# Kernel tuning notes

Measured on AMD Instinct MI355X. Metric: run time of the kernel, lower is better.

## Reference

```python
import jax, jax.numpy as jnp
import numpy as np

N = 20000          # nodes
E = 320000         # directed edges (self-loops added in reference)
F_IN = 128         # input node features
HEADS = 8
HID = 64           # per-head hidden channels
G = 64             # graphs in the batch
NUM_CLASSES = 10
NEG_SLOPE = 0.2    # PyG GATConv LeakyReLU slope


def _gat_layer(x, src, dst, W, a_src, a_dst, bias, n_nodes):
    """PyG-style GATConv: messages flow src->dst, softmax over incoming edges."""
    H, C = a_src.shape
    h = (x @ W).reshape(n_nodes, H, C)                     # [N,H,C]
    asrc = jnp.einsum('nhc,hc->nh', h, a_src)              # [N,H]
    adst = jnp.einsum('nhc,hc->nh', h, a_dst)              # [N,H]
    e = jax.nn.leaky_relu(asrc[src] + adst[dst], NEG_SLOPE)  # [Etot,H]
    emax = jax.ops.segment_max(e, dst, num_segments=n_nodes)  # [N,H]
    ee = jnp.exp(e - emax[dst])
    denom = jax.ops.segment_sum(ee, dst, num_segments=n_nodes)
    alpha = ee / (denom[dst] + 1e-16)                      # [Etot,H]
    out = jax.ops.segment_sum(h[src] * alpha[:, :, None], dst, num_segments=n_nodes)
    return out.reshape(n_nodes, H * C) + bias


def setup_inputs() -> dict:
    key = jax.random.key(0)
    ks = jax.random.split(key, 10)
    x = jax.random.normal(ks[0], (N, F_IN), jnp.float32)
    edge_index = jax.random.randint(ks[1], (2, E), 0, N, jnp.int32)
    batch = jnp.sort(jax.random.randint(ks[2], (N,), 0, G, jnp.int32))
    # layer 1: F_IN -> HEADS*HID (concat)
    W1 = jax.random.normal(ks[3], (F_IN, HEADS * HID), jnp.float32) / np.float32(np.sqrt(F_IN))
    a_src1 = jax.random.normal(ks[4], (HEADS, HID), jnp.float32) / np.float32(np.sqrt(HID))
    a_dst1 = jax.random.normal(ks[5], (HEADS, HID), jnp.float32) / np.float32(np.sqrt(HID))
    b1 = jnp.zeros((HEADS * HID,), jnp.float32)
    # layer 2: HEADS*HID -> NUM_CLASSES (1 head)
    W2 = jax.random.normal(ks[6], (HEADS * HID, NUM_CLASSES), jnp.float32) / np.float32(np.sqrt(HEADS * HID))
    a_src2 = jax.random.normal(ks[7], (1, NUM_CLASSES), jnp.float32) / np.float32(np.sqrt(NUM_CLASSES))
    a_dst2 = jax.random.normal(ks[8], (1, NUM_CLASSES), jnp.float32) / np.float32(np.sqrt(NUM_CLASSES))
    b2 = jnp.zeros((NUM_CLASSES,), jnp.float32)
    return {"x": x, "edge_index": edge_index, "batch": batch,
            "W1": W1, "a_src1": a_src1, "a_dst1": a_dst1, "b1": b1,
            "W2": W2, "a_src2": a_src2, "a_dst2": a_dst2, "b2": b2}


def reference(x, edge_index, batch, W1, a_src1, a_dst1, b1, W2, a_src2, a_dst2, b2):
    n = x.shape[0]
    loop = jnp.arange(n, dtype=edge_index.dtype)   # add_self_loops=True (PyG default)
    src = jnp.concatenate([edge_index[0], loop])
    dst = jnp.concatenate([edge_index[1], loop])
    h = jax.nn.elu(_gat_layer(x, src, dst, W1, a_src1, a_dst1, b1, n))
    h = _gat_layer(h, src, dst, W2, a_src2, a_dst2, b2, n)
    # PowerMeanAggregation with default p=1.0 == mean pooling per graph
    sums = jax.ops.segment_sum(h, batch, num_segments=G)                    # [G,NC]
    counts = jax.ops.segment_sum(jnp.ones((n, 1), h.dtype), batch, num_segments=G)
    return sums / jnp.maximum(counts, 1.0)
```

## Files before the change

kernel.cpp:

```cpp
#include <hip/hip_runtime.h>
#include <hip/hip_bf16.h>

typedef unsigned short ushort_t;
typedef unsigned int uint_t;
typedef unsigned char uchar_t;

typedef __attribute__((ext_vector_type(8))) short bf16x8;
typedef __attribute__((ext_vector_type(4))) float f32x4;
typedef __attribute__((ext_vector_type(2))) float f32x2;

__device__ __forceinline__ float bf2f(ushort_t u) {
    union { uint_t i; float f; } v; v.i = ((uint_t)u) << 16; return v.f;
}
__device__ __forceinline__ ushort_t f2bf(float f) {
    __hip_bfloat16 h = __float2bfloat16(f);
    ushort_t u; __builtin_memcpy(&u, &h, 2); return u;
}
__device__ __forceinline__ float leaky(float v) { return (v > 0.f) ? v : 0.2f * v; }

#define PO_AS1 0
#define PO_AD1 512
#define PO_B1  1024
#define PO_W2  1536
#define PO_AS2 6656
#define PO_AD2 6666
#define PO_B2  6676
#define PTOT   6686

__device__ __forceinline__ bool detect_fp32_local(const ushort_t* __restrict__ xa) {
    __shared__ int cnt;
    if (threadIdx.x == 0) cnt = 0;
    __syncthreads();
    int bad = 0;
    for (int i = threadIdx.x; i < 4096; i += 256) {
        float v = bf2f(xa[i]);
        if (!(fabsf(v) < 1e4f)) bad++;
    }
    if (bad) atomicAdd(&cnt, bad);
    __syncthreads();
    return cnt >= 16;
}

__global__ __launch_bounds__(256) void k_prep(const void* __restrict__ x,
                                              const void* __restrict__ W1,
                                              const void* as1, const void* ad1,
                                              const void* b1, const void* W2,
                                              const void* as2, const void* ad2,
                                              const void* b2,
                                              ushort_t* __restrict__ W1t,
                                              float* __restrict__ prm,
                                              float* __restrict__ vab,
                                              int* __restrict__ deg,
                                              float* __restrict__ gacc,
                                              int* __restrict__ flag, int N) {
    int b = blockIdx.x, t = threadIdx.x;
    if (b < 283) {
        bool isf = detect_fp32_local((const ushort_t*)x);
        if (b == 0 && t == 0) *flag = isf ? 1 : 0;
        if (b < 256) {
            int idx = b * 256 + t;
            int n = idx & 511, k = idx >> 9;
            float v = isf ? ((const float*)W1)[k * 512 + n]
                          : bf2f(((const ushort_t*)W1)[k * 512 + n]);
            W1t[n * 128 + k] = f2bf(v);
        } else {
            int i = (b - 256) * 256 + t;
            if (i < PTOT) {
                const void* src; int off;
                if (i < 512)       { src = as1; off = i; }
                else if (i < 1024) { src = ad1; off = i - 512; }
                else if (i < 1536) { src = b1;  off = i - 1024; }
                else if (i < 6656) { src = W2;  off = i - 1536; }
                else if (i < 6666) { src = as2; off = i - 6656; }
                else if (i < 6676) { src = ad2; off = i - 6666; }
                else               { src = b2;  off = i - 6676; }
                prm[i] = isf ? ((const float*)src)[off] : bf2f(((const ushort_t*)src)[off]);
            }
        }
    } else if (b < 362) {
        int i = (b - 283) * 256 + t;
        if (i < N) deg[i] = 0;
    } else if (b == 362) {
        for (int i = t; i < 768; i += 256) gacc[i] = 0.f;
    } else {
        bool isf = detect_fp32_local((const ushort_t*)x);
        int idx = (b - 363) * 256 + t;
        int k = idx >> 4, q = idx & 15;
        int h = q & 7;
        const void* av = (q < 8) ? as1 : ad1;
        float s = 0.f;
        for (int c = 0; c < 64; ++c) {
            float wv = isf ? ((const float*)W1)[k * 512 + h * 64 + c]
                           : bf2f(((const ushort_t*)W1)[k * 512 + h * 64 + c]);
            float aval = isf ? ((const float*)av)[h * 64 + c]
                             : bf2f(((const ushort_t*)av)[h * 64 + c]);
            s += wv * aval;
        }
        vab[k * 16 + q] = s;
    }
}

__global__ __launch_bounds__(256) void k_logits_hist(const void* __restrict__ xraw,
                                                     const float* __restrict__ vab,
                                                     const int* __restrict__ ei,
                                                     const int* __restrict__ flag,
                                                     uchar_t* __restrict__ xq,
                                                     float* __restrict__ asrcf,
                                                     float* __restrict__ adstf,
                                                     int* __restrict__ deg,
                                                     int E, int Etot) {
    int b = blockIdx.x, t = threadIdx.x;
    if (b >= 1250) {
        int e = (b - 1250) * 256 + t;
        if (e < Etot) {
            int dst = (e < E) ? ei[E + e] : (e - E);
            atomicAdd(&deg[dst], 1);
        }
        return;
    }
    bool isf = (*flag != 0);
    int n = b * 16 + (t >> 4);
    int l = t & 15;
    int ch0 = l * 8;
    float xf[8];
    if (isf) {
        const float4* x4 = (const float4*)xraw + (size_t)n * 32 + l * 2;
        float4 f0 = x4[0], f1 = x4[1];
        xf[0] = f0.x; xf[1] = f0.y; xf[2] = f0.z; xf[3] = f0.w;
        xf[4] = f1.x; xf[5] = f1.y; xf[6] = f1.z; xf[7] = f1.w;
    } else {
        uint4 u = ((const uint4*)((const ushort_t*)xraw + (size_t)n * 128))[l];
        xf[0] = bf2f(u.x & 0xffff); xf[1] = bf2f(u.x >> 16);
        xf[2] = bf2f(u.y & 0xffff); xf[3] = bf2f(u.y >> 16);
        xf[4] = bf2f(u.z & 0xffff); xf[5] = bf2f(u.z >> 16);
        xf[6] = bf2f(u.w & 0xffff); xf[7] = bf2f(u.w >> 16);
    }
    uint_t u0 = (uint_t)__builtin_amdgcn_cvt_pk_fp8_f32(xf[0], xf[1], 0, false);
    u0 = (uint_t)__builtin_amdgcn_cvt_pk_fp8_f32(xf[2], xf[3], (int)u0, true);
    uint_t u1 = (uint_t)__builtin_amdgcn_cvt_pk_fp8_f32(xf[4], xf[5], 0, false);
    u1 = (uint_t)__builtin_amdgcn_cvt_pk_fp8_f32(xf[6], xf[7], (int)u1, true);
    uint2 st; st.x = u0; st.y = u1;
    *((uint2*)(xq + (size_t)n * 128) + l) = st;
    float ps[8], pd[8];
#pragma unroll
    for (int h = 0; h < 8; ++h) { ps[h] = 0.f; pd[h] = 0.f; }
#pragma unroll
    for (int j = 0; j < 8; ++j) {
        const float4* vr = (const float4*)&vab[(ch0 + j) * 16];
        float4 va0 = vr[0], va1 = vr[1], vb0 = vr[2], vb1 = vr[3];
        float xv = xf[j];
        ps[0] += xv * va0.x; ps[1] += xv * va0.y; ps[2] += xv * va0.z; ps[3] += xv * va0.w;
        ps[4] += xv * va1.x; ps[5] += xv * va1.y; ps[6] += xv * va1.z; ps[7] += xv * va1.w;
        pd[0] += xv * vb0.x; pd[1] += xv * vb0.y; pd[2] += xv * vb0.z; pd[3] += xv * vb0.w;
        pd[4] += xv * vb1.x; pd[5] += xv * vb1.y; pd[6] += xv * vb1.z; pd[7] += xv * vb1.w;
    }
#pragma unroll
    for (int off = 1; off <= 8; off <<= 1) {
#pragma unroll
        for (int h = 0; h < 8; ++h) {
            ps[h] += __shfl_xor(ps[h], off, 64);
            pd[h] += __shfl_xor(pd[h], off, 64);
        }
    }
    if (l == 0) {
#pragma unroll
        for (int h = 0; h < 8; ++h) {
            asrcf[n * 8 + h] = ps[h];
            adstf[n * 8 + h] = pd[h];
        }
    }
}

__global__ __launch_bounds__(256) void k_scan(const int* __restrict__ deg,
                                              int* __restrict__ rowptr,
                                              int* __restrict__ cursor, int N) {
    int b = blockIdx.x, t = threadIdx.x;
    int lane = t & 63, wv = t >> 6;
    __shared__ int ws[4], wt[4];
    __shared__ int sbase;
    int limit = b * 256;
    int p0 = 0, p1 = 0, p2 = 0, p3 = 0;
    int i = t;
    for (; i + 768 < limit; i += 1024) {
        p0 += deg[i]; p1 += deg[i + 256]; p2 += deg[i + 512]; p3 += deg[i + 768];
    }
    for (; i < limit; i += 256) p0 += deg[i];
    int partial = (p0 + p1) + (p2 + p3);
#pragma unroll
    for (int off = 32; off; off >>= 1) partial += __shfl_xor(partial, off, 64);
    if (lane == 0) ws[wv] = partial;
    __syncthreads();
    if (t == 0) sbase = ws[0] + ws[1] + ws[2] + ws[3];
    __syncthreads();
    int base = sbase;
    i = limit + t;
    int v = (i < N) ? deg[i] : 0;
    int inc = v;
#pragma unroll
    for (int off = 1; off < 64; off <<= 1) {
        int u = __shfl_up(inc, off, 64);
        if (lane >= off) inc += u;
    }
    if (lane == 63) wt[wv] = inc;
    __syncthreads();
    int woff = 0;
    for (int w = 0; w < 4; ++w) if (w < wv) woff += wt[w];
    int excl = base + woff + inc - v;
    if (i < N) { rowptr[i + 1] = excl + v; cursor[i] = excl; }
    if (i == 0) rowptr[0] = 0;
}

__global__ __launch_bounds__(256) void k_scatter(const int* __restrict__ ei,
                                                 int* __restrict__ cursor,
                                                 const float* __restrict__ asrcf,
                                                 const float* __restrict__ adstf,
                                                 int* __restrict__ csr_src,
                                                 float* __restrict__ wcsr,
                                                 int E, int Etot) {
    int e = blockIdx.x * 256 + threadIdx.x;
    if (e >= Etot) return;
    int src, dst;
    if (e < E) { src = ei[e]; dst = ei[E + e]; } else { src = dst = e - E; }
    int pos = atomicAdd(&cursor[dst], 1);
    csr_src[pos] = src;
    const float4* ap = (const float4*)&asrcf[(size_t)src * 8];
    const float4* bp = (const float4*)&adstf[(size_t)dst * 8];
    float4 a0 = ap[0], a1 = ap[1];
    float4 b0 = bp[0], b1 = bp[1];
    float4 w0, w1;
    w0.x = __expf(leaky(a0.x + b0.x));
    w0.y = __expf(leaky(a0.y + b0.y));
    w0.z = __expf(leaky(a0.z + b0.z));
    w0.w = __expf(leaky(a0.w + b0.w));
    w1.x = __expf(leaky(a1.x + b1.x));
    w1.y = __expf(leaky(a1.y + b1.y));
    w1.z = __expf(leaky(a1.z + b1.z));
    w1.w = __expf(leaky(a1.w + b1.w));
    float4* wp = (float4*)&wcsr[(size_t)pos * 8];
    wp[0] = w0; wp[1] = w1;
}

__global__ __launch_bounds__(256) void k_aggfused(const uchar_t* __restrict__ xq,
                                                  const int* __restrict__ rowptr,
                                                  const int* __restrict__ csr_src,
                                                  const float* __restrict__ wcsr,
                                                  const ushort_t* __restrict__ w1t,
                                                  const float* __restrict__ prm,
                                                  ushort_t* __restrict__ h2,
                                                  float* __restrict__ asrc2f,
                                                  float* __restrict__ adst2f) {
    __shared__ ushort_t sA[16 * 1040];
    int b = blockIdx.x, t = threadIdx.x;
    int m0 = b * 16;
    int wave = t >> 6, lane = t & 63;
    for (int mm = 0; mm < 4; ++mm) {
        int mloc = wave * 4 + mm;
        int n = m0 + mloc;
        int start = rowptr[n], end = rowptr[n + 1];
        float acc[16];
        float den[8];
#pragma unroll
        for (int i = 0; i < 16; ++i) acc[i] = 0.f;
#pragma unroll
        for (int h = 0; h < 8; ++h) den[h] = 0.f;
        for (int base = start; base < end; base += 64) {
            int mcap = min(64, end - base);
            int sIdx = csr_src[base + min(lane, mcap - 1)];
            for (int g = 0; g < mcap; g += 4) {
                int s[4]; float4 wA[4], wB[4]; ushort_t xv[4];
#pragma unroll
                for (int j = 0; j < 4; ++j)
                    s[j] = __shfl(sIdx, min(g + j, mcap - 1), 64);
#pragma unroll
                for (int j = 0; j < 4; ++j) {
                    const float4* wp = (const float4*)&wcsr[(size_t)(base + min(g + j, mcap - 1)) * 8];
                    wA[j] = wp[0]; wB[j] = wp[1];
                }
#pragma unroll
                for (int j = 0; j < 4; ++j)
                    xv[j] = *(const ushort_t*)&xq[(size_t)s[j] * 128 + lane * 2];
#pragma unroll
                for (int j = 0; j < 4; ++j) {
                    float msk = (g + j < mcap) ? 1.f : 0.f;
                    f32x2 q = __builtin_amdgcn_cvt_pk_f32_fp8((int)xv[j], false);
                    float w0 = wA[j].x * msk, w1 = wA[j].y * msk, w2 = wA[j].z * msk, w3 = wA[j].w * msk;
                    float w4 = wB[j].x * msk, w5 = wB[j].y * msk, w6 = wB[j].z * msk, w7 = wB[j].w * msk;
                    den[0] += w0; acc[0]  += w0 * q.x; acc[1]  += w0 * q.y;
                    den[1] += w1; acc[2]  += w1 * q.x; acc[3]  += w1 * q.y;
                    den[2] += w2; acc[4]  += w2 * q.x; acc[5]  += w2 * q.y;
                    den[3] += w3; acc[6]  += w3 * q.x; acc[7]  += w3 * q.y;
                    den[4] += w4; acc[8]  += w4 * q.x; acc[9]  += w4 * q.y;
                    den[5] += w5; acc[10] += w5 * q.x; acc[11] += w5 * q.y;
                    den[6] += w6; acc[12] += w6 * q.x; acc[13] += w6 * q.y;
                    den[7] += w7; acc[14] += w7 * q.x; acc[15] += w7 * q.y;
                }
            }
        }
#pragma unroll
        for (int h = 0; h < 8; ++h) {
            float inv = 1.f / (den[h] + 1e-16f);
            uint_t u = (uint_t)f2bf(acc[2 * h] * inv) | ((uint_t)f2bf(acc[2 * h + 1] * inv) << 16);
            *(uint_t*)&sA[mloc * 1040 + h * 128 + 2 * lane] = u;
        }
    }
    __syncthreads();
    int mr = lane & 15, quad = lane >> 4;
    int n0 = wave * 128;
    f32x4 acc2[8];
#pragma unroll
    for (int ct = 0; ct < 8; ++ct) acc2[ct] = {0.f, 0.f, 0.f, 0.f};
#pragma unroll
    for (int kk = 0; kk < 4; ++kk) {
        bf16x8 a0 = *reinterpret_cast<const bf16x8*>(
            &sA[mr * 1040 + (wave * 2) * 128 + quad * 8 + kk * 32]);
        bf16x8 a1 = *reinterpret_cast<const bf16x8*>(
            &sA[mr * 1040 + (wave * 2 + 1) * 128 + quad * 8 + kk * 32]);
#pragma unroll
        for (int ct = 0; ct < 8; ++ct) {
            bf16x8 bb = *reinterpret_cast<const bf16x8*>(
                &w1t[(size_t)(n0 + ct * 16 + mr) * 128 + quad * 8 + kk * 32]);
            acc2[ct] = __builtin_amdgcn_mfma_f32_16x16x32_bf16(ct < 4 ? a0 : a1, bb, acc2[ct], 0, 0, 0);
        }
    }
    __syncthreads();
    ushort_t* h1s = sA;
    int col = lane & 15;
#pragma unroll
    for (int ct = 0; ct < 8; ++ct) {
        int abscol = n0 + ct * 16 + col;
        float bb1 = prm[PO_B1 + abscol];
#pragma unroll
        for (int r = 0; r < 4; ++r) {
            float v = acc2[ct][r] + bb1;
            v = (v > 0.f) ? v : expm1f(v);
            h1s[(quad * 4 + r) * 512 + abscol] = f2bf(v);
        }
    }
    __syncthreads();
    int cb = lane * 8;
    for (int mm = 0; mm < 4; ++mm) {
        int m = wave * 4 + mm;
        int n = m0 + m;
        bf16x8 hv = *reinterpret_cast<const bf16x8*>(&h1s[m * 512 + cb]);
        float p2[10];
#pragma unroll
        for (int c = 0; c < 10; ++c) p2[c] = 0.f;
#pragma unroll
        for (int j = 0; j < 8; ++j) {
            float rv = bf2f((ushort_t)hv[j]);
            const float2* wrow = reinterpret_cast<const float2*>(&prm[PO_W2 + (cb + j) * 10]);
            float2 w01 = wrow[0], w23 = wrow[1], w45 = wrow[2], w67 = wrow[3], w89 = wrow[4];
            p2[0] += rv * w01.x; p2[1] += rv * w01.y;
            p2[2] += rv * w23.x; p2[3] += rv * w23.y;
            p2[4] += rv * w45.x; p2[5] += rv * w45.y;
            p2[6] += rv * w67.x; p2[7] += rv * w67.y;
            p2[8] += rv * w89.x; p2[9] += rv * w89.y;
        }
#pragma unroll
        for (int c = 0; c < 10; ++c)
#pragma unroll
            for (int off = 32; off; off >>= 1)
                p2[c] += __shfl_xor(p2[c], off, 64);
        if (lane == 0) {
            float as = 0.f, ad = 0.f;
#pragma unroll
            for (int c = 0; c < 10; ++c) {
                h2[(size_t)n * 16 + c] = f2bf(p2[c]);
                as += p2[c] * prm[PO_AS2 + c];
                ad += p2[c] * prm[PO_AD2 + c];
            }
            asrc2f[n] = as; adst2f[n] = ad;
        }
    }
}

__global__ __launch_bounds__(256) void k_agg2f(const ushort_t* __restrict__ h2,
                                               const float* __restrict__ asrc2f,
                                               const float* __restrict__ adst2f,
                                               const int* __restrict__ rowptr,
                                               const int* __restrict__ csr_src,
                                               const float* __restrict__ prm,
                                               const int* __restrict__ batch,
                                               float* __restrict__ gacc,
                                               float* __restrict__ gcnt,
                                               int* __restrict__ donecnt,
                                               const int* __restrict__ flag,
                                               void* __restrict__ dout) {
    int t = threadIdx.x;
    int grp = t >> 4, l = t & 15;
    int n = blockIdx.x * 16 + grp;
    int start = rowptr[n], end = rowptr[n + 1];
    float adn = adst2f[n];
    float den = 0.f;
    float oc[10];
#pragma unroll
    for (int c = 0; c < 10; ++c) oc[c] = 0.f;
    for (int e = start + l; e < end; e += 16) {
        int s = csr_src[e];
        float lo = asrc2f[s];
        const uint_t* hp = (const uint_t*)(h2 + (size_t)s * 16);
        uint4 ha = *(const uint4*)hp;
        uint_t hb = hp[4];
        float ee = __expf(leaky(lo + adn));
        den += ee;
        oc[0] += ee * bf2f(ha.x & 0xffff); oc[1] += ee * bf2f(ha.x >> 16);
        oc[2] += ee * bf2f(ha.y & 0xffff); oc[3] += ee * bf2f(ha.y >> 16);
        oc[4] += ee * bf2f(ha.z & 0xffff); oc[5] += ee * bf2f(ha.z >> 16);
        oc[6] += ee * bf2f(ha.w & 0xffff); oc[7] += ee * bf2f(ha.w >> 16);
        oc[8] += ee * bf2f(hb & 0xffff);   oc[9] += ee * bf2f(hb >> 16);
    }
#pragma unroll
    for (int off = 8; off; off >>= 1) {
        den += __shfl_xor(den, off, 64);
#pragma unroll
        for (int c = 0; c < 10; ++c) oc[c] += __shfl_xor(oc[c], off, 64);
    }
    __shared__ float sres[16][12];
    __shared__ int sg[16];
    if (l == 0) {
        float invd = 1.f / (den + 1e-16f);
#pragma unroll
        for (int c = 0; c < 10; ++c) sres[grp][c] = oc[c] * invd + prm[PO_B2 + c];
        sres[grp][10] = 1.f;
        sg[grp] = batch[n];
    }
    __syncthreads();
    if (t < 11) {
        int c = t;
        float run = sres[0][c]; int g = sg[0];
        for (int k = 1; k < 16; ++k) {
            if (sg[k] != g) {
                atomicAdd(c < 10 ? &gacc[g * 10 + c] : &gcnt[g], run);
                g = sg[k]; run = 0.f;
            }
            run += sres[k][c];
        }
        atomicAdd(c < 10 ? &gacc[g * 10 + c] : &gcnt[g], run);
    }
    __syncthreads();
    __shared__ int slast;
    if (t == 0) {
        __threadfence();
        int d = atomicAdd(donecnt, 1);
        slast = (d == (int)gridDim.x - 1) ? 1 : 0;
    }
    __syncthreads();
    if (slast && t < 64) {
        __threadfence();
        bool isf = (*flag != 0);
        const volatile float* ga = (const volatile float*)gacc;
        const volatile float* gc = (const volatile float*)gcnt;
        float cnt = fmaxf(gc[t], 1.f);
        for (int c = 0; c < 10; ++c) {
            float r = ga[t * 10 + c] / cnt;
            if (isf) ((float*)dout)[t * 10 + c] = r;
            else     ((ushort_t*)dout)[t * 10 + c] = f2bf(r);
        }
    }
}

extern "C" void kernel_launch(void* const* d_in, const int* in_sizes, int n_in,
                              void* d_out, int out_size, void* d_ws, size_t ws_size,
                              hipStream_t stream) {
    const void* x   = d_in[0];
    const int* ei   = (const int*)d_in[1];
    const int* batch= (const int*)d_in[2];
    const void* W1  = d_in[3];
    const void* as1 = d_in[4];
    const void* ad1 = d_in[5];
    const void* b1  = d_in[6];
    const void* W2  = d_in[7];
    const void* as2 = d_in[8];
    const void* ad2 = d_in[9];
    const void* b2  = d_in[10];

    constexpr int N = 20000, E = 320000, Etot = E + N;
    constexpr int histBlocks = (Etot + 255) / 256;

    char* p = (char*)d_ws;
    auto alloc = [&](size_t bytes) {
        char* r = p; p += (bytes + 255) & ~(size_t)255; return r;
    };
    int* flag       = (int*)alloc(256);
    float* prm      = (float*)alloc((size_t)PTOT * 4);
    float* vab      = (float*)alloc(2048 * 4);
    ushort_t* w1t   = (ushort_t*)alloc(512 * 128 * 2);
    uchar_t* xq     = (uchar_t*)alloc((size_t)N * 128);
    float* asrc1f   = (float*)alloc((size_t)N * 8 * 4);
    float* adst1f   = (float*)alloc((size_t)N * 8 * 4);
    float* asrc2f   = (float*)alloc((size_t)N * 4);
    float* adst2f   = (float*)alloc((size_t)N * 4);
    ushort_t* h2    = (ushort_t*)alloc((size_t)N * 16 * 2);
    float* gacc     = (float*)alloc((size_t)768 * 4);
    int* deg        = (int*)alloc((size_t)N * 4);
    int* rowptr     = (int*)alloc((size_t)(N + 1) * 4);
    int* cursor     = (int*)alloc((size_t)N * 4);
    int* csr_src    = (int*)alloc((size_t)(Etot + 64) * 4);
    float* wcsr     = (float*)alloc(((size_t)Etot * 8 + 1024) * 4);
    float* gcnt     = gacc + 640;
    int* donecnt    = (int*)(gacc + 704);

    k_prep<<<371, 256, 0, stream>>>(x, W1, as1, ad1, b1, W2, as2, ad2, b2,
                                    w1t, prm, vab, deg, gacc, flag, N);
    k_logits_hist<<<1250 + histBlocks, 256, 0, stream>>>(x, vab, ei, flag, xq,
                                                         asrc1f, adst1f, deg, E, Etot);
    k_scan<<<(N + 255) / 256, 256, 0, stream>>>(deg, rowptr, cursor, N);
    k_scatter<<<histBlocks, 256, 0, stream>>>(ei, cursor, asrc1f, adst1f,
                                              csr_src, wcsr, E, Etot);
    k_aggfused<<<1250, 256, 0, stream>>>(xq, rowptr, csr_src, wcsr, w1t, prm,
                                         h2, asrc2f, adst2f);
    k_agg2f<<<N / 16, 256, 0, stream>>>(h2, asrc2f, adst2f, rowptr, csr_src, prm,
                                        batch, gacc, gcnt, donecnt, flag, d_out);
}
```

Baseline: 257.7 us.

## Restructure fused aggregation to one node per wave, add nontemporal CSR stores

```diff
diff --git a/kernel.cpp b/kernel.cpp
--- a/kernel.cpp
+++ b/kernel.cpp
@@ -222,12 +222,12 @@
     int src, dst;
     if (e < E) { src = ei[e]; dst = ei[E + e]; } else { src = dst = e - E; }
     int pos = atomicAdd(&cursor[dst], 1);
-    csr_src[pos] = src;
+    __builtin_nontemporal_store(src, &csr_src[pos]);
     const float4* ap = (const float4*)&asrcf[(size_t)src * 8];
     const float4* bp = (const float4*)&adstf[(size_t)dst * 8];
     float4 a0 = ap[0], a1 = ap[1];
     float4 b0 = bp[0], b1 = bp[1];
-    float4 w0, w1;
+    f32x4 w0, w1;
     w0.x = __expf(leaky(a0.x + b0.x));
     w0.y = __expf(leaky(a0.y + b0.y));
     w0.z = __expf(leaky(a0.z + b0.z));
@@ -236,11 +236,12 @@
     w1.y = __expf(leaky(a1.y + b1.y));
     w1.z = __expf(leaky(a1.z + b1.z));
     w1.w = __expf(leaky(a1.w + b1.w));
-    float4* wp = (float4*)&wcsr[(size_t)pos * 8];
-    wp[0] = w0; wp[1] = w1;
-}
-
-__global__ __launch_bounds__(256) void k_aggfused(const uchar_t* __restrict__ xq,
+    f32x4* wp = (f32x4*)&wcsr[(size_t)pos * 8];
+    __builtin_nontemporal_store(w0, wp);
+    __builtin_nontemporal_store(w1, wp + 1);
+}
+
+__global__ __launch_bounds__(512) void k_aggfused(const uchar_t* __restrict__ xq,
                                                   const int* __restrict__ rowptr,
                                                   const int* __restrict__ csr_src,
                                                   const float* __restrict__ wcsr,
@@ -249,13 +250,12 @@
                                                   ushort_t* __restrict__ h2,
                                                   float* __restrict__ asrc2f,
                                                   float* __restrict__ adst2f) {
-    __shared__ ushort_t sA[16 * 1040];
+    __shared__ ushort_t sA[8 * 1040];
     int b = blockIdx.x, t = threadIdx.x;
-    int m0 = b * 16;
+    int m0 = b * 8;
     int wave = t >> 6, lane = t & 63;
-    for (int mm = 0; mm < 4; ++mm) {
-        int mloc = wave * 4 + mm;
-        int n = m0 + mloc;
+    {
+        int n = m0 + wave;
         int start = rowptr[n], end = rowptr[n + 1];
         float acc[16];
         float den[8];
@@ -300,48 +300,54 @@
         for (int h = 0; h < 8; ++h) {
             float inv = 1.f / (den[h] + 1e-16f);
             uint_t u = (uint_t)f2bf(acc[2 * h] * inv) | ((uint_t)f2bf(acc[2 * h + 1] * inv) << 16);
-            *(uint_t*)&sA[mloc * 1040 + h * 128 + 2 * lane] = u;
+            *(uint_t*)&sA[wave * 1040 + h * 128 + 2 * lane] = u;
         }
     }
     __syncthreads();
     int mr = lane & 15, quad = lane >> 4;
-    int n0 = wave * 128;
     f32x4 acc2[8];
 #pragma unroll
     for (int ct = 0; ct < 8; ++ct) acc2[ct] = {0.f, 0.f, 0.f, 0.f};
-#pragma unroll
-    for (int kk = 0; kk < 4; ++kk) {
-        bf16x8 a0 = *reinterpret_cast<const bf16x8*>(
-            &sA[mr * 1040 + (wave * 2) * 128 + quad * 8 + kk * 32]);
-        bf16x8 a1 = *reinterpret_cast<const bf16x8*>(
-            &sA[mr * 1040 + (wave * 2 + 1) * 128 + quad * 8 + kk * 32]);
+    if (wave < 4) {
+        int row = mr & 7;
+#pragma unroll
+        for (int kk = 0; kk < 4; ++kk) {
+            bf16x8 a0 = *reinterpret_cast<const bf16x8*>(
+                &sA[row * 1040 + (wave * 2) * 128 + quad * 8 + kk * 32]);
+            bf16x8 a1 = *reinterpret_cast<const bf16x8*>(
+                &sA[row * 1040 + (wave * 2 + 1) * 128 + quad * 8 + kk * 32]);
+            int n0 = wave * 128;
+#pragma unroll
+            for (int ct = 0; ct < 8; ++ct) {
+                bf16x8 bb = *reinterpret_cast<const bf16x8*>(
+                    &w1t[(size_t)(n0 + ct * 16 + mr) * 128 + quad * 8 + kk * 32]);
+                acc2[ct] = __builtin_amdgcn_mfma_f32_16x16x32_bf16(ct < 4 ? a0 : a1, bb, acc2[ct], 0, 0, 0);
+            }
+        }
+    }
+    __syncthreads();
+    ushort_t* h1s = sA;
+    if (wave < 4 && quad < 2) {
+        int col = lane & 15;
+        int n0 = wave * 128;
 #pragma unroll
         for (int ct = 0; ct < 8; ++ct) {
-            bf16x8 bb = *reinterpret_cast<const bf16x8*>(
-                &w1t[(size_t)(n0 + ct * 16 + mr) * 128 + quad * 8 + kk * 32]);
-            acc2[ct] = __builtin_amdgcn_mfma_f32_16x16x32_bf16(ct < 4 ? a0 : a1, bb, acc2[ct], 0, 0, 0);
-        }
-    }
-    __syncthreads();
-    ushort_t* h1s = sA;
-    int col = lane & 15;
-#pragma unroll
-    for (int ct = 0; ct < 8; ++ct) {
-        int abscol = n0 + ct * 16 + col;
-        float bb1 = prm[PO_B1 + abscol];
-#pragma unroll
-        for (int r = 0; r < 4; ++r) {
-            float v = acc2[ct][r] + bb1;
-            v = (v > 0.f) ? v : expm1f(v);
-            h1s[(quad * 4 + r) * 512 + abscol] = f2bf(v);
-        }
-    }
-    __syncthreads();
-    int cb = lane * 8;
-    for (int mm = 0; mm < 4; ++mm) {
-        int m = wave * 4 + mm;
-        int n = m0 + m;
-        bf16x8 hv = *reinterpret_cast<const bf16x8*>(&h1s[m * 512 + cb]);
+            int abscol = n0 + ct * 16 + col;
+            float bb1 = prm[PO_B1 + abscol];
+#pragma unroll
+            for (int r = 0; r < 4; ++r) {
+                int rowi = quad * 4 + r;
+                float v = acc2[ct][r] + bb1;
+                v = (v > 0.f) ? v : expm1f(v);
+                h1s[rowi * 512 + abscol] = f2bf(v);
+            }
+        }
+    }
+    __syncthreads();
+    {
+        int n = m0 + wave;
+        int cb = lane * 8;
+        bf16x8 hv = *reinterpret_cast<const bf16x8*>(&h1s[wave * 512 + cb]);
         float p2[10];
 #pragma unroll
         for (int c = 0; c < 10; ++c) p2[c] = 0.f;
@@ -507,8 +513,8 @@
     k_scan<<<(N + 255) / 256, 256, 0, stream>>>(deg, rowptr, cursor, N);
     k_scatter<<<histBlocks, 256, 0, stream>>>(ei, cursor, asrc1f, adst1f,
                                               csr_src, wcsr, E, Etot);
-    k_aggfused<<<1250, 256, 0, stream>>>(xq, rowptr, csr_src, wcsr, w1t, prm,
-                                         h2, asrc2f, adst2f);
+    k_aggfused<<<N / 8, 512, 0, stream>>>(xq, rowptr, csr_src, wcsr, w1t, prm,
+                                          h2, asrc2f, adst2f);
     k_agg2f<<<N / 16, 256, 0, stream>>>(h2, asrc2f, adst2f, rowptr, csr_src, prm,
                                         batch, gacc, gcnt, donecnt, flag, d_out);
 }
```

Result: slower. 316.9 us (+23.0%).
